# Kernel tuning notes

Hardware: AMD Instinct MI355X
Metric: run time of the kernel (lower is better)

The kernel has to match this reference:

```python
import jax, jax.numpy as jnp
import numpy as np
from jax import lax

WS = 8          # window size
HEADS = 8
DIM = 192       # embed_dim == v_dim inside block
HD = DIM // HEADS
SCALE = HD ** -0.5
EPS = 1e-5


def _rel_pos_index(ws):
    coords = np.stack(np.meshgrid(np.arange(ws), np.arange(ws), indexing='ij'))  # (2,ws,ws)
    cf = coords.reshape(2, -1)                       # (2, n)
    rel = (cf[:, :, None] - cf[:, None, :]).transpose(1, 2, 0).astype(np.int64)  # (n,n,2)
    rel[..., 0] += ws - 1
    rel[..., 1] += ws - 1
    rel[..., 0] *= 2 * ws - 1
    return rel.sum(-1)                               # (n, n) int


def _ln(x, w, b):
    m = jnp.mean(x, axis=-1, keepdims=True)
    v = jnp.mean(jnp.square(x - m), axis=-1, keepdims=True)
    return (x - m) * lax.rsqrt(v + EPS) * w + b


def _conv3x3(x, w, b):
    y = lax.conv_general_dilated(x, w, (1, 1), ((1, 1), (1, 1)),
                                 dimension_numbers=('NCHW', 'OIHW', 'NCHW'))
    return y + b[None, :, None, None]


def setup_inputs():
    key = jax.random.key(0)
    ks = jax.random.split(key, 24)
    f = lambda k, shape: (jax.random.normal(k, shape, jnp.float32) * 0.02)
    inp = {
        'x': jax.random.normal(ks[0], (8, 96, 128, 128), jnp.float32),
        'v': jax.random.normal(ks[1], (8, 96, 128, 128), jnp.float32),
        'pq_w': f(ks[2], (DIM, 96, 3, 3)), 'pq_b': f(ks[3], (DIM,)),
        'pv_w': f(ks[4], (DIM, 96, 3, 3)), 'pv_b': f(ks[5], (DIM,)),
        'n1_w': jnp.ones((DIM,)), 'n1_b': jnp.zeros((DIM,)),
        'n2_w': jnp.ones((DIM,)), 'n2_b': jnp.zeros((DIM,)),
        'n3_w': jnp.ones((DIM,)), 'n3_b': jnp.zeros((DIM,)),
        'n4_w': jnp.ones((DIM,)), 'n4_b': jnp.zeros((DIM,)),
        'q_w': f(ks[6], (DIM, DIM)),
        'kv_w': f(ks[7], (2 * DIM, DIM)),
        'ap_w': f(ks[8], (DIM, DIM)), 'ap_b': f(ks[9], (DIM,)),
        'rpb': f(ks[10], ((2 * WS - 1) * (2 * WS - 1), HEADS)),
        'fc1_w': f(ks[11], (4 * DIM, DIM)), 'fc1_b': f(ks[12], (4 * DIM,)),
        'fc2_w': f(ks[13], (DIM, 4 * DIM)), 'fc2_b': f(ks[14], (DIM,)),
    }
    return inp


def reference(x, v, pq_w, pq_b, pv_w, pv_b, n1_w, n1_b, n2_w, n2_b, n3_w, n3_b,
              n4_w, n4_b, q_w, kv_w, ap_w, ap_b, rpb, fc1_w, fc1_b, fc2_w, fc2_b):
    # conv projections (input_dim != embed_dim, v_dim != embed_dim)
    x = _conv3x3(x, pq_w, pq_b)
    v = _conv3x3(v, pv_w, pv_b)
    x_proj, v_proj = x, v
    b, c, h, w = x.shape
    n = WS * WS

    xs = _ln(x.reshape(b, c, h * w).transpose(0, 2, 1), n1_w, n1_b).reshape(b, h, w, c)
    vs = _ln(v.reshape(b, c, h * w).transpose(0, 2, 1), n2_w, n2_b).reshape(b, h, w, c)

    pad_r = (WS - w % WS) % WS
    pad_b_ = (WS - h % WS) % WS
    if pad_r or pad_b_:
        xs = jnp.pad(xs, ((0, 0), (0, pad_b_), (0, pad_r), (0, 0)))
        vs = jnp.pad(vs, ((0, 0), (0, pad_b_), (0, pad_r), (0, 0)))
    hp, wp = h + pad_b_, w + pad_r

    def partition(t):  # (b,hp,wp,c) -> (nw, n, c)
        t = t.reshape(b, hp // WS, WS, wp // WS, WS, c)
        return t.transpose(0, 1, 3, 2, 4, 5).reshape(-1, n, c)

    xw = partition(xs)
    vw = partition(vs)

    # cross-window attention
    q = (xw @ q_w.T).reshape(-1, n, HEADS, HD).transpose(0, 2, 1, 3) * SCALE  # (nw,H,n,hd)
    kv = (vw @ kv_w.T).reshape(-1, n, 2, HEADS, HD).transpose(2, 0, 3, 1, 4)
    k, vv = kv[0], kv[1]                                                     # (nw,H,n,hd)
    attn = jnp.einsum('whqd,whkd->whqk', q, k)
    rel_idx = _rel_pos_index(WS)                                             # static (n,n)
    bias = rpb[rel_idx.reshape(-1)].reshape(n, n, HEADS).transpose(2, 0, 1)  # (H,n,n)
    attn = jax.nn.softmax(attn + bias[None], axis=-1)
    out = jnp.einsum('whqk,whkd->whqd', attn, vv).transpose(0, 2, 1, 3).reshape(-1, n, c)
    out = out @ ap_w.T + ap_b                                                # (nw,n,c)

    # window reverse + crop
    out = out.reshape(b, hp // WS, wp // WS, WS, WS, c).transpose(0, 1, 3, 2, 4, 5)
    out = out.reshape(b, hp, wp, c)[:, :h, :w, :].reshape(b, h * w, c)

    # mlp: note original does x = mlp(norm3(x)); x = x + drop_path(x) -> 2*mlp_out
    m = _ln(out, n3_w, n3_b)
    m = jax.nn.gelu(m @ fc1_w.T + fc1_b, approximate=False) @ fc2_w.T + fc2_b
    m = m + m
    m = _ln(m, n4_w, n4_b)
    m = m.reshape(b, h, w, c).transpose(0, 3, 1, 2)
    return m + x_proj + v_proj
```

## Files before the change

### kernel.cpp

```cpp
#include <hip/hip_runtime.h>
#include <hip/hip_bf16.h>
#include <math.h>

typedef _Float16 f16;
typedef _Float16 half8 __attribute__((ext_vector_type(8)));
typedef float f32x4 __attribute__((ext_vector_type(4)));

#define IMG 128
#define CIN 96
#define CH  192
#define SCALE_Q 0.2041241452319315f

__device__ __forceinline__ f32x4 mfma16(half8 a, half8 b, f32x4 c) {
  return __builtin_amdgcn_mfma_f32_16x16x32_f16(a, b, c, 0, 0, 0);
}

template <bool WH>
__device__ __forceinline__ half8 loadW(const void* W, int row, int k, int ldk) {
  if constexpr (WH) {
    return *(const half8*)((const f16*)W + (size_t)row * ldk + k);
  } else {
    const float* p = (const float*)W + (size_t)row * ldk + k;
    const float4 a = *(const float4*)p;
    const float4 b = *(const float4*)(p + 4);
    half8 h;
    h[0] = (f16)a.x; h[1] = (f16)a.y; h[2] = (f16)a.z; h[3] = (f16)a.w;
    h[4] = (f16)b.x; h[5] = (f16)b.y; h[6] = (f16)b.z; h[7] = (f16)b.w;
    return h;
  }
}

__device__ __forceinline__ float gelu(float x) {
  const float u = 0.70710678118654752f * x;
  const float a = fabsf(u);
  const float t = 1.0f / (1.0f + 0.3275911f * a);
  const float poly = t * (0.254829592f + t * (-0.284496736f +
                     t * (1.421413741f + t * (-1.453152027f + t * 1.061405429f))));
  float er = 1.0f - poly * __expf(-u * u);
  er = (u < 0.f) ? -er : er;
  return 0.5f * x * (1.0f + er);
}

__global__ __launch_bounds__(256) void reorder_w(
    const float* __restrict__ pq_w, const float* __restrict__ pv_w,
    const float* __restrict__ qW, const float* __restrict__ kvW,
    f16* __restrict__ Wr, f16* __restrict__ wq16) {
  const int i = blockIdx.x * 256 + threadIdx.x;
  if (i < 2 * 192 * 864) {
    const int which = i / (192 * 864);
    const int rem = i - which * (192 * 864);
    const int co = rem / 864;
    const int kk = rem - co * 864;
    const int s = kk / 96;
    const int ci = kk - s * 96;
    const float* src = which ? pv_w : pq_w;
    Wr[i] = (f16)src[co * 864 + ci * 9 + s];
  } else if (wq16) {
    const int j = i - 2 * 192 * 864;
    if (j < 110592)
      wq16[j] = (f16)(j < 36864 ? qW[j] : kvW[j - 36864]);
  }
}

__global__ __launch_bounds__(256) void reorder_w2(
    const float* __restrict__ apW, const float* __restrict__ w1,
    const float* __restrict__ w2, f16* __restrict__ dst) {
  const int i = blockIdx.x * 256 + threadIdx.x;
  if (i >= 331776) return;
  float v;
  if (i < 36864)       v = apW[i];
  else if (i < 184320) v = w1[i - 36864];
  else                 v = w2[i - 184320];
  dst[i] = (f16)v;
}

__global__ __launch_bounds__(256, 2) void conv3x3_mfma(
    const float* __restrict__ xin, const float* __restrict__ vin,
    const f16* __restrict__ Wr,
    const float* __restrict__ pq_b, const float* __restrict__ pv_b,
    f16* __restrict__ xp, f16* __restrict__ vp) {
  int bz = blockIdx.x;
  const int which = bz >> 10; bz &= 1023;
  const int b = bz >> 7;
  const int yp = (bz >> 1) & 63;
  const int xseg = bz & 1;
  const int y0 = yp * 2;
  const int x0 = xseg * 64;
  const float* in = which ? vin : xin;
  const float* bias = which ? pv_b : pq_b;
  const f16* W = Wr + (size_t)which * 192 * 864;
  f16* out = which ? vp : xp;

  __shared__ __align__(16) f16 ST[4 * 66 * 104];
  const int tid = threadIdx.x;
  for (int i = tid; i < 4 * 96 * 66; i += 256) {
    const int r = i / 6336;
    const int rem2 = i - r * 6336;
    const int c = rem2 / 66;
    const int xx = rem2 - c * 66;
    const int gy = y0 + r - 1;
    const int gx = x0 - 1 + xx;
    float val = 0.f;
    if (gy >= 0 && gy < IMG && gx >= 0 && gx < IMG)
      val = in[(((size_t)b * CIN + c) * IMG + gy) * IMG + gx];
    ST[(r * 66 + xx) * 104 + c] = (f16)val;
  }
  __syncthreads();

  const int lane = tid & 63;
  const int wv = tid >> 6;
  const int l15 = lane & 15;
  const int quad = lane >> 4;
  const int nb = wv * 48;

  f32x4 acc[8][3];
  #pragma unroll
  for (int mt = 0; mt < 8; ++mt)
    #pragma unroll
    for (int j = 0; j < 3; ++j) acc[mt][j] = (f32x4)0.f;

  #pragma unroll
  for (int s = 0; s < 9; ++s) {
    const int ky = s / 3, kx = s - ky * 3;
    #pragma unroll
    for (int kstep = 0; kstep < 3; ++kstep) {
      const int k = kstep * 32 + quad * 8;
      half8 a[8];
      #pragma unroll
      for (int mt = 0; mt < 8; ++mt)
        a[mt] = *(const half8*)(ST + (((mt >> 2) + ky) * 66 + (mt & 3) * 16 + l15 + kx) * 104 + k);
      #pragma unroll
      for (int j = 0; j < 3; ++j) {
        const half8 bf = *(const half8*)(W + (size_t)(nb + j * 16 + l15) * 864 + s * 96 + k);
        #pragma unroll
        for (int mt = 0; mt < 8; ++mt) acc[mt][j] = mfma16(a[mt], bf, acc[mt][j]);
      }
    }
  }

  #pragma unroll
  for (int j = 0; j < 3; ++j) {
    const int n = nb + j * 16 + l15;
    const float bn = bias[n];
    #pragma unroll
    for (int mt = 0; mt < 8; ++mt) {
      const int row = y0 + (mt >> 2);
      const int px = x0 + (mt & 3) * 16 + quad * 4;
      const int tok = (b * IMG + row) * IMG + px;
      #pragma unroll
      for (int reg = 0; reg < 4; ++reg)
        out[(size_t)(tok + reg) * CH + n] = (f16)(acc[mt][j][reg] + bn);
    }
  }
}

template <bool WH>
__global__ __launch_bounds__(256, 1) void ln_qkv_mfma(
    f16* __restrict__ xp, const f16* __restrict__ vp,
    const float* __restrict__ n1w, const float* __restrict__ n1b,
    const float* __restrict__ n2w, const float* __restrict__ n2b,
    const void* __restrict__ qW, const void* __restrict__ kvW,
    f16* __restrict__ qb, f16* __restrict__ kb, f16* __restrict__ vb) {
  const int tid = threadIdx.x;
  const int lane = tid & 63;
  const int wv = tid >> 6;
  const int l15 = lane & 15;
  const int quad = lane >> 4;
  const int tok0 = blockIdx.x * 32;
  __shared__ __align__(16) f16 Ax[32 * 200];
  __shared__ __align__(16) f16 Av[32 * 200];

  {
    const int r = tid >> 3;
    const int s = tid & 7;
    const size_t gbase = (size_t)(tok0 + r) * 192 + s * 24;
    half8 hx[3], hv[3];
    const half8* px = (const half8*)(xp + gbase);
    const half8* pv = (const half8*)(vp + gbase);
    #pragma unroll
    for (int i = 0; i < 3; ++i) { hx[i] = px[i]; hv[i] = pv[i]; }
    float xv[24], vvv[24];
    float sx = 0.f, sx2 = 0.f, sv = 0.f, sv2 = 0.f;
    #pragma unroll
    for (int i = 0; i < 24; ++i) {
      xv[i] = (float)hx[i >> 3][i & 7];
      vvv[i] = (float)hv[i >> 3][i & 7];
      sx += xv[i]; sx2 += xv[i] * xv[i];
      sv += vvv[i]; sv2 += vvv[i] * vvv[i];
    }
    half8 hr[3];
    #pragma unroll
    for (int i = 0; i < 24; ++i) hr[i >> 3][i & 7] = (f16)(xv[i] + vvv[i]);
    half8* pr = (half8*)(xp + gbase);
    #pragma unroll
    for (int i = 0; i < 3; ++i) pr[i] = hr[i];
    #pragma unroll
    for (int m = 1; m < 8; m <<= 1) {
      sx += __shfl_xor(sx, m, 64); sx2 += __shfl_xor(sx2, m, 64);
      sv += __shfl_xor(sv, m, 64); sv2 += __shfl_xor(sv2, m, 64);
    }
    const float mx = sx * (1.f / 192.f);
    const float rx = rsqrtf(sx2 * (1.f / 192.f) - mx * mx + 1e-5f);
    const float mv = sv * (1.f / 192.f);
    const float rv = rsqrtf(sv2 * (1.f / 192.f) - mv * mv + 1e-5f);
    #pragma unroll
    for (int i = 0; i < 24; ++i) {
      const int c = s * 24 + i;
      Ax[r * 200 + c] = (f16)((xv[i] - mx) * rx * n1w[c] + n1b[c]);
      Av[r * 200 + c] = (f16)((vvv[i] - mv) * rv * n2w[c] + n2b[c]);
    }
  }
  __syncthreads();

  const int nb = wv * 144;
  f32x4 acc[2][9];
  #pragma unroll
  for (int mt = 0; mt < 2; ++mt)
    #pragma unroll
    for (int j = 0; j < 9; ++j) acc[mt][j] = (f32x4)0.f;

  for (int kc = 0; kc < 6; ++kc) {
    const int k = kc * 32 + quad * 8;
    half8 wb[9];
    #pragma unroll
    for (int j = 0; j < 9; ++j) {
      const int n0 = nb + j * 16;
      if (n0 < 192) wb[j] = loadW<WH>(qW, n0 + l15, k, 192);
      else          wb[j] = loadW<WH>(kvW, n0 - 192 + l15, k, 192);
    }
    const half8 ax0 = *(const half8*)(Ax + l15 * 200 + k);
    const half8 ax1 = *(const half8*)(Ax + (16 + l15) * 200 + k);
    const half8 av0 = *(const half8*)(Av + l15 * 200 + k);
    const half8 av1 = *(const half8*)(Av + (16 + l15) * 200 + k);
    #pragma unroll
    for (int j = 0; j < 9; ++j) {
      const int n0 = nb + j * 16;
      if (n0 < 192) {
        acc[0][j] = mfma16(ax0, wb[j], acc[0][j]);
        acc[1][j] = mfma16(ax1, wb[j], acc[1][j]);
      } else {
        acc[0][j] = mfma16(av0, wb[j], acc[0][j]);
        acc[1][j] = mfma16(av1, wb[j], acc[1][j]);
      }
    }
  }

  int wro[8];
  #pragma unroll
  for (int mt = 0; mt < 2; ++mt)
    #pragma unroll
    for (int reg = 0; reg < 4; ++reg) {
      const int tok = tok0 + mt * 16 + quad * 4 + reg;
      const int bb = tok >> 14;
      const int y = (tok >> 7) & 127;
      const int xx = tok & 127;
      const int wi = bb * 256 + ((y >> 3) << 4) + (xx >> 3);
      const int t = (y & 7) * 8 + (xx & 7);
      wro[mt * 4 + reg] = wi * 12288 + t * 24;
    }
  #pragma unroll
  for (int j = 0; j < 9; ++j) {
    const int n = nb + j * 16 + l15;
    f16* dst; int c; float scale = 1.f;
    if (n < 192)      { dst = qb; c = n;       scale = SCALE_Q; }
    else if (n < 384) { dst = kb; c = n - 192; }
    else              { dst = vb; c = n - 384; }
    const int h = c / 24;
    const int cof = h * 1536 + (c - h * 24);
    #pragma unroll
    for (int mt = 0; mt < 2; ++mt)
      #pragma unroll
      for (int reg = 0; reg < 4; ++reg)
        dst[wro[mt * 4 + reg] + cof] = (f16)(acc[mt][j][reg] * scale);
  }
}

__global__ __launch_bounds__(64) void attn64(
    const f16* __restrict__ qb, const f16* __restrict__ kb,
    const f16* __restrict__ vb, const float* __restrict__ rpb,
    f16* __restrict__ fb) {
  const int wh = blockIdx.x;
  const int h = wh & 7;
  const int w = wh >> 3;
  const int t = threadIdx.x;
  __shared__ __align__(16) float ks[64 * 24];
  __shared__ __align__(16) float vs[64 * 24];
  __shared__ float bsh[225];
  const f16* kbase = kb + (size_t)wh * 1536;
  const f16* vbase = vb + (size_t)wh * 1536;
  for (int i = t; i < 1536; i += 64) { ks[i] = (float)kbase[i]; vs[i] = (float)vbase[i]; }
  for (int i = t; i < 225; i += 64) bsh[i] = rpb[i * 8 + h];
  float q[24];
  const f16* qrow = qb + ((size_t)wh * 64 + t) * 24;
  #pragma unroll
  for (int d = 0; d < 24; ++d) q[d] = (float)qrow[d];
  __syncthreads();
  const int qy = t >> 3, qx = t & 7;
  float s[64];
  float mx = -1e30f;
  #pragma unroll
  for (int kk = 0; kk < 64; ++kk) {
    float acc = 0.f;
    #pragma unroll
    for (int d = 0; d < 24; ++d) acc += q[d] * ks[kk * 24 + d];
    const int ky = kk >> 3, kx = kk & 7;
    acc += bsh[(qy - ky + 7) * 15 + (qx - kx + 7)];
    s[kk] = acc;
    mx = fmaxf(mx, acc);
  }
  float sum = 0.f;
  #pragma unroll
  for (int kk = 0; kk < 64; ++kk) { const float e = __expf(s[kk] - mx); s[kk] = e; sum += e; }
  const float inv = 1.0f / sum;
  float o[24];
  #pragma unroll
  for (int d = 0; d < 24; ++d) o[d] = 0.f;
  #pragma unroll
  for (int kk = 0; kk < 64; ++kk) {
    const float p = s[kk];
    #pragma unroll
    for (int d = 0; d < 24; ++d) o[d] += p * vs[kk * 24 + d];
  }
  f16* orow = fb + ((size_t)w * 64 + t) * 192 + h * 24;
  #pragma unroll
  for (int d = 0; d < 24; ++d) orow[d] = (f16)(o[d] * inv);
}

__global__ __launch_bounds__(256, 1) void ap_ln3_mfma(
    f16* __restrict__ fb, const f16* __restrict__ apW,
    const float* __restrict__ apb,
    const float* __restrict__ n3w, const float* __restrict__ n3b) {
  const int tid = threadIdx.x;
  const int lane = tid & 63;
  const int wv = tid >> 6;
  const int l15 = lane & 15;
  const int quad = lane >> 4;
  const int wt0 = blockIdx.x * 64;
  __shared__ __align__(16) f16 As[64 * 200];
  __shared__ float rs[64], rq[64];
  if (tid < 64) { rs[tid] = 0.f; rq[tid] = 0.f; }
  for (int i = tid; i < 64 * 24; i += 256) {
    const int r = i / 24, s = i - r * 24;
    *(half8*)(As + r * 200 + s * 8) = *(const half8*)(fb + (size_t)(wt0 + r) * 192 + s * 8);
  }
  __syncthreads();

  const int nb = wv * 48;
  f32x4 acc[4][3];
  #pragma unroll
  for (int mt = 0; mt < 4; ++mt)
    #pragma unroll
    for (int j = 0; j < 3; ++j) acc[mt][j] = (f32x4)0.f;

  #pragma unroll
  for (int g = 0; g < 2; ++g) {
    half8 wb[3][3];
    #pragma unroll
    for (int u = 0; u < 3; ++u) {
      const int k = (g * 3 + u) * 32 + quad * 8;
      #pragma unroll
      for (int j = 0; j < 3; ++j)
        wb[u][j] = *(const half8*)(apW + (size_t)(nb + j * 16 + l15) * 192 + k);
    }
    #pragma unroll
    for (int u = 0; u < 3; ++u) {
      const int k = (g * 3 + u) * 32 + quad * 8;
      half8 a[4];
      #pragma unroll
      for (int mt = 0; mt < 4; ++mt)
        a[mt] = *(const half8*)(As + (mt * 16 + l15) * 200 + k);
      #pragma unroll
      for (int j = 0; j < 3; ++j)
        #pragma unroll
        for (int mt = 0; mt < 4; ++mt) acc[mt][j] = mfma16(a[mt], wb[u][j], acc[mt][j]);
    }
  }
  float bias[3];
  #pragma unroll
  for (int j = 0; j < 3; ++j) bias[j] = apb[nb + j * 16 + l15];
  #pragma unroll
  for (int mt = 0; mt < 4; ++mt)
    #pragma unroll
    for (int j = 0; j < 3; ++j)
      #pragma unroll
      for (int reg = 0; reg < 4; ++reg) acc[mt][j][reg] += bias[j];

  float ssum[16], ssq[16];
  #pragma unroll
  for (int mt = 0; mt < 4; ++mt)
    #pragma unroll
    for (int reg = 0; reg < 4; ++reg) {
      const int i = mt * 4 + reg;
      const float a0 = acc[mt][0][reg], a1 = acc[mt][1][reg], a2 = acc[mt][2][reg];
      ssum[i] = a0 + a1 + a2;
      ssq[i] = a0 * a0 + a1 * a1 + a2 * a2;
    }
  #pragma unroll
  for (int m = 1; m < 16; m <<= 1)
    #pragma unroll
    for (int i = 0; i < 16; ++i) {
      ssum[i] += __shfl_xor(ssum[i], m, 64);
      ssq[i] += __shfl_xor(ssq[i], m, 64);
    }
  if (l15 == 0) {
    #pragma unroll
    for (int mt = 0; mt < 4; ++mt)
      #pragma unroll
      for (int reg = 0; reg < 4; ++reg) {
        const int row = mt * 16 + quad * 4 + reg;
        atomicAdd(&rs[row], ssum[mt * 4 + reg]);
        atomicAdd(&rq[row], ssq[mt * 4 + reg]);
      }
  }
  __syncthreads();

  float w3[3], b3[3]; int cc[3];
  #pragma unroll
  for (int j = 0; j < 3; ++j) {
    cc[j] = nb + j * 16 + l15;
    w3[j] = n3w[cc[j]]; b3[j] = n3b[cc[j]];
  }
  #pragma unroll
  for (int mt = 0; mt < 4; ++mt)
    #pragma unroll
    for (int reg = 0; reg < 4; ++reg) {
      const int row = mt * 16 + quad * 4 + reg;
      const float mean = rs[row] * (1.f / 192.f);
      const float rstd = rsqrtf(rq[row] * (1.f / 192.f) - mean * mean + 1e-5f);
      #pragma unroll
      for (int j = 0; j < 3; ++j)
        fb[(size_t)(wt0 + row) * 192 + cc[j]] =
            (f16)((acc[mt][j][reg] - mean) * rstd * w3[j] + b3[j]);
    }
}

__global__ __launch_bounds__(256, 2) void mlp_mfma(
    const f16* __restrict__ m, const f16* __restrict__ w1,
    const float* __restrict__ b1, const f16* __restrict__ w2,
    const float* __restrict__ b2,
    const float* __restrict__ n4w, const float* __restrict__ n4b,
    const f16* __restrict__ res, float* __restrict__ out) {
  const int tid = threadIdx.x;
  const int lane = tid & 63;
  const int wv = tid >> 6;
  const int l15 = lane & 15;
  const int quad = lane >> 4;
  const int wt0 = blockIdx.x * 32;
  __shared__ __align__(16) f16 SB[32 * 776];
  __shared__ float rs[32], rq[32];
  if (tid < 32) { rs[tid] = 0.f; rq[tid] = 0.f; }
  for (int i = tid; i < 32 * 24; i += 256) {
    const int r = i / 24, s = i - r * 24;
    *(half8*)(SB + r * 200 + s * 8) = *(const half8*)(m + (size_t)(wt0 + r) * 192 + s * 8);
  }
  __syncthreads();

  const int nb1 = wv * 192;
  f32x4 acc1[2][12];
  #pragma unroll
  for (int mt = 0; mt < 2; ++mt)
    #pragma unroll
    for (int j = 0; j < 12; ++j) acc1[mt][j] = (f32x4)0.f;
  for (int kc = 0; kc < 6; ++kc) {
    const int k = kc * 32 + quad * 8;
    half8 wb[12];
    #pragma unroll
    for (int j = 0; j < 12; ++j)
      wb[j] = *(const half8*)(w1 + (size_t)(nb1 + j * 16 + l15) * 192 + k);
    const half8 a0 = *(const half8*)(SB + l15 * 200 + k);
    const half8 a1 = *(const half8*)(SB + (16 + l15) * 200 + k);
    #pragma unroll
    for (int j = 0; j < 12; ++j) {
      acc1[0][j] = mfma16(a0, wb[j], acc1[0][j]);
      acc1[1][j] = mfma16(a1, wb[j], acc1[1][j]);
    }
  }
  __syncthreads();
  #pragma unroll
  for (int j = 0; j < 12; ++j) {
    const int n = nb1 + j * 16 + l15;
    const float bj = b1[n];
    #pragma unroll
    for (int mt = 0; mt < 2; ++mt)
      #pragma unroll
      for (int reg = 0; reg < 4; ++reg) {
        const int row = mt * 16 + quad * 4 + reg;
        SB[row * 776 + n] = (f16)gelu(acc1[mt][j][reg] + bj);
      }
  }
  __syncthreads();

  const int nb2 = wv * 48;
  int cc[3];
  #pragma unroll
  for (int j = 0; j < 3; ++j) cc[j] = nb2 + j * 16 + l15;
  const int wi = wt0 >> 6;
  const int t_base = wt0 & 63;
  const int b_img = wi >> 8;
  const int wy = (wi >> 4) & 15;
  const int wx = wi & 15;
  float rr[2][3][4];
  #pragma unroll
  for (int mt = 0; mt < 2; ++mt) {
    const int t0 = t_base + mt * 16 + quad * 4;
    const int y = wy * 8 + (t0 >> 3);
    const int xx0 = wx * 8 + (t0 & 7);
    const size_t tokbase = ((size_t)(b_img * 128 + y)) * 128 + xx0;
    #pragma unroll
    for (int j = 0; j < 3; ++j)
      #pragma unroll
      for (int reg = 0; reg < 4; ++reg)
        rr[mt][j][reg] = (float)res[(tokbase + reg) * 192 + cc[j]];
  }

  f32x4 acc2[2][3];
  #pragma unroll
  for (int mt = 0; mt < 2; ++mt)
    #pragma unroll
    for (int j = 0; j < 3; ++j) acc2[mt][j] = (f32x4)0.f;
  for (int g = 0; g < 6; ++g) {
    half8 wb[4][3];
    #pragma unroll
    for (int u = 0; u < 4; ++u) {
      const int k = (g * 4 + u) * 32 + quad * 8;
      #pragma unroll
      for (int j = 0; j < 3; ++j)
        wb[u][j] = *(const half8*)(w2 + (size_t)(nb2 + j * 16 + l15) * 768 + k);
    }
    #pragma unroll
    for (int u = 0; u < 4; ++u) {
      const int k = (g * 4 + u) * 32 + quad * 8;
      const half8 a0 = *(const half8*)(SB + l15 * 776 + k);
      const half8 a1 = *(const half8*)(SB + (16 + l15) * 776 + k);
      #pragma unroll
      for (int j = 0; j < 3; ++j) {
        acc2[0][j] = mfma16(a0, wb[u][j], acc2[0][j]);
        acc2[1][j] = mfma16(a1, wb[u][j], acc2[1][j]);
      }
    }
  }
  float w4[3], b4[3];
  #pragma unroll
  for (int j = 0; j < 3; ++j) {
    const float bj = b2[cc[j]];
    w4[j] = n4w[cc[j]]; b4[j] = n4b[cc[j]];
    #pragma unroll
    for (int mt = 0; mt < 2; ++mt)
      #pragma unroll
      for (int reg = 0; reg < 4; ++reg)
        acc2[mt][j][reg] = 2.f * (acc2[mt][j][reg] + bj);
  }
  float ssum[8], ssq[8];
  #pragma unroll
  for (int mt = 0; mt < 2; ++mt)
    #pragma unroll
    for (int reg = 0; reg < 4; ++reg) {
      const int i = mt * 4 + reg;
      const float a0 = acc2[mt][0][reg], a1 = acc2[mt][1][reg], a2 = acc2[mt][2][reg];
      ssum[i] = a0 + a1 + a2;
      ssq[i] = a0 * a0 + a1 * a1 + a2 * a2;
    }
  #pragma unroll
  for (int mm = 1; mm < 16; mm <<= 1)
    #pragma unroll
    for (int i = 0; i < 8; ++i) {
      ssum[i] += __shfl_xor(ssum[i], mm, 64);
      ssq[i] += __shfl_xor(ssq[i], mm, 64);
    }
  if (l15 == 0) {
    #pragma unroll
    for (int mt = 0; mt < 2; ++mt)
      #pragma unroll
      for (int reg = 0; reg < 4; ++reg) {
        const int row = mt * 16 + quad * 4 + reg;
        atomicAdd(&rs[row], ssum[mt * 4 + reg]);
        atomicAdd(&rq[row], ssq[mt * 4 + reg]);
      }
  }
  __syncthreads();

  #pragma unroll
  for (int mt = 0; mt < 2; ++mt) {
    const int row0 = mt * 16 + quad * 4;
    const int t0 = t_base + row0;
    const int y = wy * 8 + (t0 >> 3);
    const int x0 = wx * 8 + (t0 & 7);
    float mean[4], rstd[4];
    #pragma unroll
    for (int reg = 0; reg < 4; ++reg) {
      const int row = row0 + reg;
      mean[reg] = rs[row] * (1.f / 192.f);
      rstd[reg] = rsqrtf(rq[row] * (1.f / 192.f) - mean[reg] * mean[reg] + 1e-5f);
    }
    #pragma unroll
    for (int j = 0; j < 3; ++j) {
      float4 o;
      float vals[4];
      #pragma unroll
      for (int reg = 0; reg < 4; ++reg)
        vals[reg] = (acc2[mt][j][reg] - mean[reg]) * rstd[reg] * w4[j] + b4[j] + rr[mt][j][reg];
      o.x = vals[0]; o.y = vals[1]; o.z = vals[2]; o.w = vals[3];
      float* dst = out + ((size_t)(b_img * 192 + cc[j])) * 16384 + (y * 128 + x0);
      *(float4*)dst = o;
    }
  }
}

extern "C" void kernel_launch(void* const* d_in, const int* in_sizes, int n_in,
                              void* d_out, int out_size, void* d_ws, size_t ws_size,
                              hipStream_t stream) {
  (void)in_sizes; (void)n_in; (void)out_size;
  const float* x    = (const float*)d_in[0];
  const float* v    = (const float*)d_in[1];
  const float* pq_w = (const float*)d_in[2];
  const float* pq_b = (const float*)d_in[3];
  const float* pv_w = (const float*)d_in[4];
  const float* pv_b = (const float*)d_in[5];
  const float* n1w  = (const float*)d_in[6];
  const float* n1b  = (const float*)d_in[7];
  const float* n2w  = (const float*)d_in[8];
  const float* n2b  = (const float*)d_in[9];
  const float* n3w  = (const float*)d_in[10];
  const float* n3b  = (const float*)d_in[11];
  const float* n4w  = (const float*)d_in[12];
  const float* n4b  = (const float*)d_in[13];
  const float* qW   = (const float*)d_in[14];
  const float* kvW  = (const float*)d_in[15];
  const float* apW  = (const float*)d_in[16];
  const float* apb  = (const float*)d_in[17];
  const float* rpb  = (const float*)d_in[18];
  const float* w1   = (const float*)d_in[19];
  const float* b1   = (const float*)d_in[20];
  const float* w2   = (const float*)d_in[21];
  const float* b2   = (const float*)d_in[22];
  float* out = (float*)d_out;

  const size_t HE = 25165824;
  f16* xp   = (f16*)d_ws;
  f16* vp   = xp + HE;
  f16* vvb  = vp + HE;
  f16* qb   = (f16*)d_out;
  f16* kb   = qb + HE;
  f16* fb   = vp;
  f16* Wr   = vvb;
  f16* wtail = vvb + HE;
  const bool big = ws_size >= (3 * HE + 110592) * sizeof(f16);

  reorder_w<<<big ? 1728 : 1296, 256, 0, stream>>>(pq_w, pv_w, qW, kvW, Wr,
                                                   big ? wtail : (f16*)nullptr);
  conv3x3_mfma<<<2048, 256, 0, stream>>>(x, v, Wr, pq_b, pv_b, xp, vp);
  if (big)
    ln_qkv_mfma<true><<<4096, 256, 0, stream>>>(xp, vp, n1w, n1b, n2w, n2b,
                                                wtail, wtail + 36864, qb, kb, vvb);
  else
    ln_qkv_mfma<false><<<4096, 256, 0, stream>>>(xp, vp, n1w, n1b, n2w, n2b,
                                                 qW, kvW, qb, kb, vvb);
  attn64<<<16384, 64, 0, stream>>>(qb, kb, vvb, rpb, fb);
  reorder_w2<<<1296, 256, 0, stream>>>(apW, w1, w2, vvb);
  ap_ln3_mfma<<<2048, 256, 0, stream>>>(fb, vvb, apb, n3w, n3b);
  mlp_mfma<<<4096, 256, 0, stream>>>(fb, vvb + 36864, b1, vvb + 184320, b2,
                                     n4w, n4b, xp, out);
}
```

Measured before the change: 1.176 ms.

## Batch conv input loads and stage conv/QKV outputs through LDS for vector stores

The conv input staging loop is unrolled into batches of 11 loads, with clamped addresses and predicated zeroing, so many global loads are in flight at once. Both the conv kernel and the LN+QKV kernel now write accumulator results into shared memory first and then emit coalesced 16-byte half8 stores to global memory, replacing scattered 2-byte strided stores. This targets store inefficiency and load latency, at the cost of extra LDS traffic, added syncthreads and higher register pressure.

```diff
diff --git a/kernel.cpp b/kernel.cpp
--- a/kernel.cpp
+++ b/kernel.cpp
@@ -93,17 +93,29 @@
 
   __shared__ __align__(16) f16 ST[4 * 66 * 104];
   const int tid = threadIdx.x;
-  for (int i = tid; i < 4 * 96 * 66; i += 256) {
-    const int r = i / 6336;
-    const int rem2 = i - r * 6336;
-    const int c = rem2 / 66;
-    const int xx = rem2 - c * 66;
-    const int gy = y0 + r - 1;
-    const int gx = x0 - 1 + xx;
-    float val = 0.f;
-    if (gy >= 0 && gy < IMG && gx >= 0 && gx < IMG)
-      val = in[(((size_t)b * CIN + c) * IMG + gy) * IMG + gx];
-    ST[(r * 66 + xx) * 104 + c] = (f16)val;
+  #pragma unroll
+  for (int batch = 0; batch < 9; ++batch) {
+    float vals[11];
+    bool oks[11];
+    int sts[11];
+    #pragma unroll
+    for (int u = 0; u < 11; ++u) {
+      const int i = tid + (batch * 11 + u) * 256;
+      const int r = i / 6336;
+      const int rem2 = i - r * 6336;
+      const int c = rem2 / 66;
+      const int xx = rem2 - c * 66;
+      const int gy = y0 + r - 1;
+      const int gx = x0 - 1 + xx;
+      oks[u] = ((unsigned)gy < IMG) && ((unsigned)gx < IMG);
+      const int cgy = min(max(gy, 0), IMG - 1);
+      const int cgx = min(max(gx, 0), IMG - 1);
+      vals[u] = in[(((size_t)b * CIN + c) * IMG + cgy) * IMG + cgx];
+      sts[u] = (r * 66 + xx) * 104 + c;
+    }
+    #pragma unroll
+    for (int u = 0; u < 11; ++u)
+      ST[sts[u]] = oks[u] ? (f16)vals[u] : (f16)0.f;
   }
   __syncthreads();
 
@@ -137,6 +149,7 @@
       }
     }
   }
+  __syncthreads();
 
   #pragma unroll
   for (int j = 0; j < 3; ++j) {
@@ -144,13 +157,24 @@
     const float bn = bias[n];
     #pragma unroll
     for (int mt = 0; mt < 8; ++mt) {
-      const int row = y0 + (mt >> 2);
-      const int px = x0 + (mt & 3) * 16 + quad * 4;
-      const int tok = (b * IMG + row) * IMG + px;
+      const int lt = (mt >> 2) * 64 + (mt & 3) * 16 + quad * 4;
       #pragma unroll
       for (int reg = 0; reg < 4; ++reg)
-        out[(size_t)(tok + reg) * CH + n] = (f16)(acc[mt][j][reg] + bn);
-    }
+        ST[(lt + reg) * 204 + n] = (f16)(acc[mt][j][reg] + bn);
+    }
+  }
+  __syncthreads();
+
+  const size_t rowbase0 = ((size_t)(b * IMG + y0) * IMG + x0) * CH;
+  const size_t rowbase1 = ((size_t)(b * IMG + y0 + 1) * IMG + x0) * CH;
+  #pragma unroll
+  for (int it = 0; it < 12; ++it) {
+    const int i = tid + it * 256;
+    const int tok = i / 24, c8 = i - tok * 24;
+    const half8 hval = *(const half8*)(ST + tok * 204 + c8 * 8);
+    const int trow = tok >> 6, tx = tok & 63;
+    f16* dst = out + (trow ? rowbase1 : rowbase0) + (size_t)tx * CH + c8 * 8;
+    *(half8*)dst = hval;
   }
 }
 
@@ -167,8 +191,9 @@
   const int l15 = lane & 15;
   const int quad = lane >> 4;
   const int tok0 = blockIdx.x * 32;
-  __shared__ __align__(16) f16 Ax[32 * 200];
-  __shared__ __align__(16) f16 Av[32 * 200];
+  __shared__ __align__(16) f16 U[32 * 588];
+  f16* Ax = U;
+  f16* Av = U + 6400;
 
   {
     const int r = tid >> 3;
@@ -244,34 +269,42 @@
       }
     }
   }
-
-  int wro[8];
-  #pragma unroll
-  for (int mt = 0; mt < 2; ++mt)
-    #pragma unroll
-    for (int reg = 0; reg < 4; ++reg) {
-      const int tok = tok0 + mt * 16 + quad * 4 + reg;
-      const int bb = tok >> 14;
-      const int y = (tok >> 7) & 127;
-      const int xx = tok & 127;
-      const int wi = bb * 256 + ((y >> 3) << 4) + (xx >> 3);
-      const int t = (y & 7) * 8 + (xx & 7);
-      wro[mt * 4 + reg] = wi * 12288 + t * 24;
-    }
+  __syncthreads();
+
   #pragma unroll
   for (int j = 0; j < 9; ++j) {
     const int n = nb + j * 16 + l15;
-    f16* dst; int c; float scale = 1.f;
-    if (n < 192)      { dst = qb; c = n;       scale = SCALE_Q; }
-    else if (n < 384) { dst = kb; c = n - 192; }
-    else              { dst = vb; c = n - 384; }
-    const int h = c / 24;
-    const int cof = h * 1536 + (c - h * 24);
+    const float scale = (n < 192) ? SCALE_Q : 1.f;
     #pragma unroll
     for (int mt = 0; mt < 2; ++mt)
       #pragma unroll
-      for (int reg = 0; reg < 4; ++reg)
-        dst[wro[mt * 4 + reg] + cof] = (f16)(acc[mt][j][reg] * scale);
+      for (int reg = 0; reg < 4; ++reg) {
+        const int r = mt * 16 + quad * 4 + reg;
+        U[r * 588 + n] = (f16)(acc[mt][j][reg] * scale);
+      }
+  }
+  __syncthreads();
+
+  const int yrow = (tok0 >> 7) & 127;
+  const int bb = tok0 >> 14;
+  const int x0b = tok0 & 127;
+  const int wib = bb * 256 + ((yrow >> 3) << 4) + (x0b >> 3);
+  const int trow = (yrow & 7) * 8;
+  f16* const bufs[3] = {qb, kb, vb};
+  #pragma unroll
+  for (int it = 0; it < 9; ++it) {
+    const int i = tid + it * 256;
+    const int c24 = i % 24;
+    const int g = i / 24;
+    const int h = g & 7;
+    const int g2 = g >> 3;
+    const int wloc = g2 & 3;
+    const int buf = g2 >> 2;
+    const int t8 = c24 / 3, c3 = c24 - t8 * 3;
+    const int r = wloc * 8 + t8;
+    const half8 hval = *(const half8*)(U + r * 588 + buf * 192 + h * 24 + c3 * 8);
+    f16* dst = bufs[buf] + (size_t)(wib + wloc) * 12288 + (trow + t8) * 24 + h * 1536 + c3 * 8;
+    *(half8*)dst = hval;
   }
 }
 
```

Measured after the change: 1.050 ms. 10.7% less time.
